# Performance work log

Hardware: AMD Instinct MI355X
Metric: run time of the kernel (lower is better)

## Reference

```python
import jax, jax.numpy as jnp
import numpy as np

N_TERMS = 26000
N_EDGES = 120000
BATCH = 64
N_FEAT = 14          # n_base_models + 4
GO_EMB = 8
HID = 64
IN_DIM = N_FEAT + GO_EMB  # 22


def setup_inputs() -> dict:
    key = jax.random.key(0)
    ks = jax.random.split(key, 12)
    s = 0.05
    return {
        "x": jax.random.normal(ks[0], (BATCH, N_TERMS, N_FEAT), jnp.float32),
        "edge_index": jax.random.randint(ks[1], (2, N_EDGES), 0, N_TERMS, jnp.int32),
        "term_indices": jnp.arange(N_TERMS, dtype=jnp.int32),
        "emb_table": jax.random.normal(ks[2], (N_TERMS, GO_EMB), jnp.float32),
        "W1": jax.random.normal(ks[3], (HID, IN_DIM), jnp.float32) * s,
        "b1": jnp.zeros((HID,), jnp.float32),
        "W2": jax.random.normal(ks[4], (HID, HID), jnp.float32) * s,
        "b2": jnp.zeros((HID,), jnp.float32),
        "W3": jax.random.normal(ks[5], (HID // 2, HID), jnp.float32) * s,
        "b3": jnp.zeros((HID // 2,), jnp.float32),
        "Wout": jax.random.normal(ks[6], (1, HID // 2), jnp.float32) * s,
        "bout": jnp.zeros((1,), jnp.float32),
    }


def _go_conv(x, row, col, deg_inv, W, b):
    # x: [B, N, C]. Mean-aggregate neighbor features (col -> row), add self, linear.
    agg = jnp.zeros_like(x).at[:, row].add(x[:, col])        # scatter_add over edges
    agg = agg * deg_inv[None, :, None]
    return jnp.einsum('bnc,oc->bno', x + agg, W) + b


def reference(x, edge_index, term_indices, emb_table, W1, b1, W2, b2, W3, b3, Wout, bout):
    B, N, _ = x.shape
    row, col = edge_index[0], edge_index[1]
    deg = jnp.zeros((N,), x.dtype).at[row].add(1.0)
    deg_inv = 1.0 / jnp.clip(deg, 1.0)

    go_emb = emb_table[term_indices]                          # [N, GO_EMB]
    h = jnp.concatenate([x, jnp.broadcast_to(go_emb[None], (B, N, go_emb.shape[-1]))], axis=-1)

    h = jax.nn.relu(_go_conv(h, row, col, deg_inv, W1, b1))   # dropout: eval mode (identity)
    h = jax.nn.relu(_go_conv(h, row, col, deg_inv, W2, b2))
    h = jax.nn.relu(_go_conv(h, row, col, deg_inv, W3, b3))
    out = jax.nn.sigmoid(jnp.einsum('bnc,oc->bno', h, Wout) + bout)  # [B, N, 1]
    return out[..., 0]
```

## Files before the change

### kernel.cpp

```cpp
#include <hip/hip_runtime.h>
#include <stdint.h>

static constexpr int NT = 26000;
static constexpr int NE = 120000;

typedef __attribute__((ext_vector_type(8))) short short8;
typedef __attribute__((ext_vector_type(4))) float f32x4;

__device__ __forceinline__ int rfl(int v){ return __builtin_amdgcn_readfirstlane(v); }

__device__ __forceinline__ float bf_lo(uint32_t u){ union{uint32_t u; float f;} a; a.u = u<<16; return a.f; }
__device__ __forceinline__ float bf_hi(uint32_t u){ union{uint32_t u; float f;} a; a.u = u & 0xffff0000u; return a.f; }
__device__ __forceinline__ uint32_t f2b(float f){ union{float f; uint32_t u;} a; a.f=f; return (a.u + 0x7fffu + ((a.u>>16)&1u))>>16; }

__global__ __launch_bounds__(256) void k_zero_deg(int* __restrict__ deg){
  int i = blockIdx.x*256 + threadIdx.x;
  if (i < NT) deg[i] = 0;
}
__global__ __launch_bounds__(256) void k_count(const int* __restrict__ ei, int* __restrict__ deg){
  int e = blockIdx.x*256 + threadIdx.x;
  if (e < NE) atomicAdd(&deg[ei[e]], 1);
}
__global__ __launch_bounds__(1024) void k_scan(const int* __restrict__ deg, int* __restrict__ rp,
                                               int* __restrict__ cur){
  __shared__ int part[1024];
  const int t = threadIdx.x;
  const int CH = (NT + 1023)/1024;
  const int base = t*CH;
  int sum = 0;
  for (int i=0;i<CH;i++){
    int idx=base+i;
    if (idx<NT){ int d = deg[idx]; sum += (d<=4)?4:((d+3)&~3); }
  }
  part[t] = sum;
  __syncthreads();
  for (int off=1; off<1024; off<<=1){
    int v = (t>=off) ? part[t-off] : 0;
    __syncthreads();
    part[t] += v;
    __syncthreads();
  }
  int run = (t==0) ? 0 : part[t-1];
  for (int i=0;i<CH;i++){
    int idx = base+i;
    if (idx<NT){
      int d = deg[idx];
      int slot = (d<=4)?4:((d+3)&~3);
      rp[idx] = run; cur[idx] = run;
      run += slot;
    }
  }
  if (t==1023) rp[NT] = part[1023];
}
__global__ __launch_bounds__(256) void k_init(uint32_t* __restrict__ zp, uint32_t* __restrict__ cols32,
                                              float* __restrict__ scQ, float* __restrict__ scY){
  int i = blockIdx.x*256 + threadIdx.x;
  if (i < 1024) zp[i] = 0;
  else if (i < 1024 + 112004) cols32[i-1024] = 0x65906590u;
  if (i < 2){ scQ[NT*2+i] = 0.f; scY[NT*2+i] = 0.f; }
}
__global__ __launch_bounds__(256) void k_fill(const int* __restrict__ ei, int* __restrict__ cur,
                                              uint16_t* __restrict__ cols){
  int e = blockIdx.x*256 + threadIdx.x;
  if (e < NE){
    int r = ei[e];
    int pos = atomicAdd(&cur[r], 1);
    cols[pos] = (uint16_t)ei[NE + e];
  }
}
__global__ __launch_bounds__(256) void k_prepw(const float* __restrict__ W1, const float* __restrict__ W2,
                                               const float* __restrict__ W3,
                                               uint16_t* __restrict__ Wt1, uint16_t* __restrict__ Wt2,
                                               uint16_t* __restrict__ Wt3){
  for (int idx = threadIdx.x; idx < 8192; idx += 256){
    if (idx < 2048){
      int o = idx >> 5, k = idx & 31;
      Wt1[idx] = (uint16_t)((k < 22) ? f2b(W1[o*22 + k]) : 0);
    } else if (idx < 6144){
      int j = idx - 2048;
      Wt2[j] = (uint16_t)f2b(W2[j]);
    } else {
      int j = idx - 6144;
      Wt3[j] = (uint16_t)f2b(W3[j]);
    }
  }
}

__global__ __launch_bounds__(256) void k_build_h0(const float* __restrict__ x, const int* __restrict__ tidx,
                                                  const float* __restrict__ emb, uint32_t* __restrict__ h0){
  const int n  = blockIdx.x*16 + (threadIdx.x & 15);
  const int b0 = threadIdx.x >> 4;
  const float* er = emb + (size_t)tidx[n]*8;
  float ev[8];
  #pragma unroll
  for (int i=0;i<8;i++) ev[i]=er[i];
  uint32_t* dst = h0 + (size_t)n*512;

  #pragma unroll
  for (int h=0; h<2; h++){
    const int b = b0 + h*16;
    const float* xr = x + ((size_t)b*NT + n)*14;
    float v[32];
    #pragma unroll
    for (int i=0;i<14;i++) v[i]=xr[i];
    #pragma unroll
    for (int i=0;i<8;i++) v[14+i]=ev[i];
    #pragma unroll
    for (int i=22;i<32;i++) v[i]=0.f;
    uint32_t p[16];
    #pragma unroll
    for (int u=0;u<16;u++) p[u] = f2b(v[2*u]) | (f2b(v[2*u+1])<<16);
    const int base = (b>>4)*256 + (b&15)*8;
    *reinterpret_cast<uint4*>(dst + base)       = make_uint4(p[0],p[1],p[2],p[3]);
    *reinterpret_cast<uint4*>(dst + base + 4)   = make_uint4(p[4],p[5],p[6],p[7]);
    *reinterpret_cast<uint4*>(dst + base + 128)   = make_uint4(p[8],p[9],p[10],p[11]);
    *reinterpret_cast<uint4*>(dst + base + 132)   = make_uint4(p[12],p[13],p[14],p[15]);
  }
}

template<int STR>
__device__ __forceinline__ const uint32_t* nbp(const uint32_t* __restrict__ hin,
                                               const uint32_t* __restrict__ zp, int c){
  return (c < NT) ? (hin + (size_t)c*STR) : zp;
}
template<int KS>
__device__ __forceinline__ void gloadv(uint4 (&v)[KS], const uint32_t* __restrict__ p,
                                       const uint32_t (&off)[KS]){
  #pragma unroll
  for (int ks=0; ks<KS; ks++) v[ks] = *reinterpret_cast<const uint4*>(p + off[ks]);
}
template<int KS>
__device__ __forceinline__ void accum(float (&acc)[KS][8], const uint4 (&v)[KS]){
  #pragma unroll
  for (int ks=0;ks<KS;ks++){
    acc[ks][0]+=bf_lo(v[ks].x); acc[ks][1]+=bf_hi(v[ks].x);
    acc[ks][2]+=bf_lo(v[ks].y); acc[ks][3]+=bf_hi(v[ks].y);
    acc[ks][4]+=bf_lo(v[ks].z); acc[ks][5]+=bf_hi(v[ks].z);
    acc[ks][6]+=bf_lo(v[ks].w); acc[ks][7]+=bf_hi(v[ks].w);
  }
}
template<int KS, int STR>
__device__ __forceinline__ float aggregate(float (&acc)[KS][8],
    const uint32_t* __restrict__ hin, const uint32_t* __restrict__ zp,
    const int* __restrict__ rp, const int* __restrict__ cur,
    const uint16_t* __restrict__ cols, int node, const uint32_t (&off)[KS])
{
  const int e0 = rfl(rp[node]);
  const int e1 = rfl(rp[node+1]);
  const int dg = rfl(cur[node]) - e0;

  uint2 cc0 = *reinterpret_cast<const uint2*>(cols + e0);
  int q0 = rfl(cc0.x), q1 = rfl(cc0.y);
  uint4 v0[KS], v1[KS], v2[KS], v3[KS], own[KS];
  gloadv<KS>(v0, nbp<STR>(hin, zp, q0 & 0xffff), off);
  gloadv<KS>(v1, nbp<STR>(hin, zp, (q0 >> 16) & 0xffff), off);
  gloadv<KS>(v2, nbp<STR>(hin, zp, q1 & 0xffff), off);
  gloadv<KS>(v3, nbp<STR>(hin, zp, (q1 >> 16) & 0xffff), off);
  gloadv<KS>(own, hin + (size_t)node*STR, off);
  uint2 ccA = *reinterpret_cast<const uint2*>(cols + e0 + 4);

  const float degf = (float)(dg > 1 ? dg : 1);
  #pragma unroll
  for (int ks=0;ks<KS;ks++){
    acc[ks][0]=bf_lo(own[ks].x)*degf; acc[ks][1]=bf_hi(own[ks].x)*degf;
    acc[ks][2]=bf_lo(own[ks].y)*degf; acc[ks][3]=bf_hi(own[ks].y)*degf;
    acc[ks][4]=bf_lo(own[ks].z)*degf; acc[ks][5]=bf_hi(own[ks].z)*degf;
    acc[ks][6]=bf_lo(own[ks].w)*degf; acc[ks][7]=bf_hi(own[ks].w)*degf;
  }

  for (int e = e0; e < e1; e += 4){
    uint2 ccN = *reinterpret_cast<const uint2*>(cols + e + 8);
    int p0 = rfl(ccA.x), p1 = rfl(ccA.y);
    int n0 = (e+4 < e1) ? (p0 & 0xffff)         : NT;
    int n1 = (e+5 < e1) ? ((p0 >> 16) & 0xffff) : NT;
    int n2 = (e+6 < e1) ? (p1 & 0xffff)         : NT;
    int n3 = (e+7 < e1) ? ((p1 >> 16) & 0xffff) : NT;
    accum<KS>(acc, v0); gloadv<KS>(v0, nbp<STR>(hin, zp, n0), off);
    accum<KS>(acc, v1); gloadv<KS>(v1, nbp<STR>(hin, zp, n1), off);
    accum<KS>(acc, v2); gloadv<KS>(v2, nbp<STR>(hin, zp, n2), off);
    accum<KS>(acc, v3); gloadv<KS>(v3, nbp<STR>(hin, zp, n3), off);
    ccA = ccN;
  }
  return 1.0f / degf;
}

template<int KS> struct VecT;
template<> struct VecT<2>{ using T = uint4; };
template<> struct VecT<1>{ using T = uint2; };

__device__ __forceinline__ void dqu32(float* a, uint32_t u, float s){
  a[0] += s*(float)(int8_t)(u & 0xff);
  a[1] += s*(float)(int8_t)((u>>8) & 0xff);
  a[2] += s*(float)(int8_t)((u>>16) & 0xff);
  a[3] += s*(float)(int8_t)(u>>24);
}
template<int KS>
__device__ __forceinline__ void dqv(float (&acc)[KS][8], const typename VecT<KS>::T& v, float s){
  if constexpr (KS==2){
    dqu32(&acc[0][0], v.x, s); dqu32(&acc[0][4], v.y, s);
    dqu32(&acc[1][0], v.z, s); dqu32(&acc[1][4], v.w, s);
  } else {
    dqu32(&acc[0][0], v.x, s); dqu32(&acc[0][4], v.y, s);
  }
}
template<int KS, int STRB>
__device__ __forceinline__ float aggregate_i8(float (&acc)[KS][8],
    const uint8_t* __restrict__ hin, const uint8_t* __restrict__ zp8,
    const float* __restrict__ sc,
    const int* __restrict__ rp, const int* __restrict__ cur,
    const uint16_t* __restrict__ cols, int node, uint32_t offB, int rt)
{
  using V = typename VecT<KS>::T;
  const int e0 = rfl(rp[node]);
  const int e1 = rfl(rp[node+1]);
  const int dg = rfl(cur[node]) - e0;

  uint2 cc0 = *reinterpret_cast<const uint2*>(cols + e0);
  int a0 = rfl(cc0.x), a1 = rfl(cc0.y);
  int c0 = a0 & 0xffff, c1 = (a0>>16) & 0xffff, c2 = a1 & 0xffff, c3 = (a1>>16) & 0xffff;
  auto bp = [&](int c)->const uint8_t*{ return (c < NT) ? (hin + (size_t)c*STRB) : zp8; };

  V v0 = *reinterpret_cast<const V*>(bp(c0) + offB); float s0 = sc[c0*2+rt];
  V v1 = *reinterpret_cast<const V*>(bp(c1) + offB); float s1 = sc[c1*2+rt];
  V v2 = *reinterpret_cast<const V*>(bp(c2) + offB); float s2 = sc[c2*2+rt];
  V v3 = *reinterpret_cast<const V*>(bp(c3) + offB); float s3 = sc[c3*2+rt];
  V ow = *reinterpret_cast<const V*>(hin + (size_t)node*STRB + offB);
  float so = sc[node*2+rt];
  uint2 ccA = *reinterpret_cast<const uint2*>(cols + e0 + 4);

  const float degf = (float)(dg > 1 ? dg : 1);
  #pragma unroll
  for (int ks=0;ks<KS;ks++)
    #pragma unroll
    for (int j=0;j<8;j++) acc[ks][j]=0.f;
  dqv<KS>(acc, ow, so*degf);

  for (int e = e0; e < e1; e += 4){
    uint2 ccN = *reinterpret_cast<const uint2*>(cols + e + 8);
    int p0 = rfl(ccA.x), p1 = rfl(ccA.y);
    int n0 = (e+4 < e1) ? (p0 & 0xffff)         : NT;
    int n1 = (e+5 < e1) ? ((p0 >> 16) & 0xffff) : NT;
    int n2 = (e+6 < e1) ? (p1 & 0xffff)         : NT;
    int n3 = (e+7 < e1) ? ((p1 >> 16) & 0xffff) : NT;
    dqv<KS>(acc, v0, s0); v0 = *reinterpret_cast<const V*>(bp(n0) + offB); s0 = sc[n0*2+rt];
    dqv<KS>(acc, v1, s1); v1 = *reinterpret_cast<const V*>(bp(n1) + offB); s1 = sc[n1*2+rt];
    dqv<KS>(acc, v2, s2); v2 = *reinterpret_cast<const V*>(bp(n2) + offB); s2 = sc[n2*2+rt];
    dqv<KS>(acc, v3, s3); v3 = *reinterpret_cast<const V*>(bp(n3) + offB); s3 = sc[n3*2+rt];
    ccA = ccN;
  }
  return 1.0f / degf;
}

__global__ __launch_bounds__(256, 8) void k_layer1(
    const uint32_t* __restrict__ hin, uint8_t* __restrict__ qout, float* __restrict__ scQ,
    const int* __restrict__ rp, const int* __restrict__ cur,
    const uint16_t* __restrict__ cols, const uint32_t* __restrict__ zp,
    const uint16_t* __restrict__ Wt, const float* __restrict__ bias)
{
  constexpr int CIN=32, STR=16*CIN;
  const int t=threadIdx.x, lane=t&63, w=t>>6, l15=lane&15, lg=lane>>4;
  const int rt = w & 1;
  const int node = blockIdx.x*2 + (w>>1);

  uint32_t off[1];
  off[0] = (uint32_t)(rt*(CIN*8) + (lg>>1)*128 + l15*8 + (lg&1)*4);

  float acc[1][8];
  const float di = aggregate<1,STR>(acc, hin, zp, rp, cur, cols, node, off);

  short8 bfrag;
  #pragma unroll
  for (int j=0;j<8;j++) bfrag[j] = (short)f2b(acc[0][j]*di);

  float av[4][4];
  float m = 0.f;
  #pragma unroll
  for (int ot=0;ot<4;ot++){
    const int o0 = ot*16;
    short8 af = *reinterpret_cast<const short8*>(Wt + (o0 + l15)*CIN + lg*8);
    f32x4 d = *reinterpret_cast<const f32x4*>(bias + o0 + lg*4);
    d = __builtin_amdgcn_mfma_f32_16x16x32_bf16(af, bfrag, d, 0,0,0);
    #pragma unroll
    for (int j=0;j<4;j++){
      float v = fmaxf(d[j], 0.f);
      av[ot][j] = v;
      m = fmaxf(m, v);
    }
  }
  #pragma unroll
  for (int sh=1; sh<64; sh<<=1) m = fmaxf(m, __shfl_xor(m, sh, 64));
  const float inv = (m > 0.f) ? 127.0f/m : 0.f;

  uint8_t* base = qout + (size_t)node*2048 + rt*1024 + l15*64;
  #pragma unroll
  for (int ot=0;ot<4;ot++){
    uint32_t pk = 0;
    #pragma unroll
    for (int j=0;j<4;j++){
      int q = __float2int_rn(av[ot][j]*inv);
      pk |= (uint32_t)(q & 0xff) << (8*j);
    }
    uint32_t boff = ((((ot&1)<<1)|(lg>>1))<<4) + ((ot>>1)<<3) + ((lg&1)<<2);
    __builtin_nontemporal_store(pk, reinterpret_cast<uint32_t*>(base + boff));
  }
  if (lane == 0) scQ[node*2+rt] = m * (1.0f/127.0f);
}

__global__ __launch_bounds__(256, 6) void k_l2g3(
    const uint8_t* __restrict__ qin, const float* __restrict__ scQ,
    uint8_t* __restrict__ yout, float* __restrict__ scY,
    const int* __restrict__ rp, const int* __restrict__ cur,
    const uint16_t* __restrict__ cols, const uint8_t* __restrict__ zp8,
    const uint16_t* __restrict__ Wt2, const float* __restrict__ bias,
    const uint16_t* __restrict__ Wt3)
{
  __shared__ uint32_t lt[4*512];
  const int t=threadIdx.x, lane=t&63, w=t>>6, l15=lane&15, lg=lane>>4;
  const int rt = w & 1;
  const int node = blockIdx.x*2 + (w>>1);

  const uint32_t offB = (uint32_t)(rt*1024 + l15*64 + lg*16);

  float acc[2][8];
  const float di = aggregate_i8<2,2048>(acc, qin, zp8, scQ, rp, cur, cols, node, offB, rt);

  short8 bfrag[2];
  #pragma unroll
  for (int ks=0;ks<2;ks++){
    short8 bf;
    #pragma unroll
    for (int j=0;j<8;j++) bf[j] = (short)f2b(acc[ks][j]*di);
    bfrag[ks]=bf;
  }

  uint32_t* L = lt + w*512;
  #pragma unroll
  for (int ot=0;ot<4;ot++){
    const int o0 = ot*16;
    short8 af0 = *reinterpret_cast<const short8*>(Wt2 + (o0 + l15)*64 + lg*8);
    short8 af1 = *reinterpret_cast<const short8*>(Wt2 + (o0 + l15)*64 + 32 + lg*8);
    f32x4 d = *reinterpret_cast<const f32x4*>(bias + o0 + lg*4);
    d = __builtin_amdgcn_mfma_f32_16x16x32_bf16(af0, bfrag[0], d, 0,0,0);
    d = __builtin_amdgcn_mfma_f32_16x16x32_bf16(af1, bfrag[1], d, 0,0,0);
    float a0=fmaxf(d[0],0.f), a1=fmaxf(d[1],0.f), a2=fmaxf(d[2],0.f), a3=fmaxf(d[3],0.f);
    *reinterpret_cast<uint2*>(L + ot*128 + l15*8 + lg*2) =
        make_uint2(f2b(a0) | (f2b(a1)<<16), f2b(a2) | (f2b(a3)<<16));
  }

  short8 b3f[2];
  #pragma unroll
  for (int ks=0;ks<2;ks++)
    b3f[ks] = *reinterpret_cast<const short8*>(L + (ks*2+(lg>>1))*128 + l15*8 + (lg&1)*4);

  float dd[2][4];
  float m = 0.f;
  #pragma unroll
  for (int ot=0;ot<2;ot++){
    const int o0 = ot*16;
    short8 af0 = *reinterpret_cast<const short8*>(Wt3 + (o0 + l15)*64 + lg*8);
    short8 af1 = *reinterpret_cast<const short8*>(Wt3 + (o0 + l15)*64 + 32 + lg*8);
    f32x4 d = {0.f,0.f,0.f,0.f};
    d = __builtin_amdgcn_mfma_f32_16x16x32_bf16(af0, b3f[0], d, 0,0,0);
    d = __builtin_amdgcn_mfma_f32_16x16x32_bf16(af1, b3f[1], d, 0,0,0);
    #pragma unroll
    for (int j=0;j<4;j++){
      dd[ot][j] = d[j];
      m = fmaxf(m, fabsf(d[j]));
    }
  }
  #pragma unroll
  for (int sh=1; sh<64; sh<<=1) m = fmaxf(m, __shfl_xor(m, sh, 64));
  const float inv = (m > 0.f) ? 127.0f/m : 0.f;

  uint8_t* base = yout + (size_t)node*1024 + rt*512 + l15*32;
  #pragma unroll
  for (int ot=0;ot<2;ot++){
    uint32_t pk = 0;
    #pragma unroll
    for (int j=0;j<4;j++){
      int q = __float2int_rn(dd[ot][j]*inv);
      pk |= (uint32_t)(q & 0xff) << (8*j);
    }
    uint32_t boff = (((ot<<1)|(lg>>1))<<3) + ((lg&1)<<2);
    __builtin_nontemporal_store(pk, reinterpret_cast<uint32_t*>(base + boff));
  }
  if (lane == 0) scY[node*2+rt] = m * (1.0f/127.0f);
}

__global__ __launch_bounds__(256, 8) void k_fin(
    const uint8_t* __restrict__ yin, const float* __restrict__ scY,
    const int* __restrict__ rp, const int* __restrict__ cur,
    const uint16_t* __restrict__ cols, const uint8_t* __restrict__ zp8,
    const float* __restrict__ b3, const float* __restrict__ Wo, const float* __restrict__ bo,
    float* __restrict__ tmp)
{
  const int t=threadIdx.x, lane=t&63, w=t>>6, l15=lane&15, lg=lane>>4;
  const int rt = w & 1;
  const int node = blockIdx.x*2 + (w>>1);

  const uint32_t offB = (uint32_t)(rt*512 + l15*32 + lg*8);

  float acc[1][8];
  const float di = aggregate_i8<1,1024>(acc, yin, zp8, scY, rp, cur, cols, node, offB, rt);

  const int k0 = lg*8;
  f32x4 bA = *reinterpret_cast<const f32x4*>(b3 + k0);
  f32x4 bB = *reinterpret_cast<const f32x4*>(b3 + k0 + 4);
  f32x4 wA = *reinterpret_cast<const f32x4*>(Wo + k0);
  f32x4 wB = *reinterpret_cast<const f32x4*>(Wo + k0 + 4);
  float z = 0.f;
  #pragma unroll
  for (int j=0;j<4;j++){
    z += fmaxf(acc[0][j]  *di + bA[j], 0.f) * wA[j];
    z += fmaxf(acc[0][4+j]*di + bB[j], 0.f) * wB[j];
  }
  z += __shfl_xor(z, 16, 64);
  z += __shfl_xor(z, 32, 64);
  if (lg == 0){
    float sg = 1.f/(1.f + expf(-(z + bo[0])));
    tmp[(size_t)node*32 + rt*16 + l15] = sg;
  }
}

__global__ __launch_bounds__(256) void k_tr(const float* __restrict__ tmp, float* __restrict__ out){
  int n = blockIdx.x*256 + threadIdx.x;
  if (n < NT){
    f32x4 r[8];
    #pragma unroll
    for (int q=0;q<8;q++) r[q] = *reinterpret_cast<const f32x4*>(tmp + (size_t)n*32 + q*4);
    #pragma unroll
    for (int q=0;q<8;q++)
      #pragma unroll
      for (int j=0;j<4;j++)
        out[(size_t)(q*4+j)*NT + n] = r[q][j];
  }
}

static constexpr size_t OFF_P    = 0;
static constexpr size_t OFF_Q    = 53248000;
static constexpr size_t OFF_TMP  = 106496000;
static constexpr size_t OFF_ZP   = 109824000;
static constexpr size_t OFF_WT1  = OFF_ZP  + 4096;
static constexpr size_t OFF_WT2  = OFF_WT1 + 4096;
static constexpr size_t OFF_WT3  = OFF_WT2 + 8192;
static constexpr size_t OFF_SCQ  = OFF_WT3 + 4096;
static constexpr size_t OFF_SCY  = OFF_SCQ + 208016;
static constexpr size_t OFF_DEG  = OFF_SCY + 208016;
static constexpr size_t OFF_RP   = OFF_DEG + 104000;
static constexpr size_t OFF_CUR  = OFF_RP  + 104016;
static constexpr size_t OFF_COLS = OFF_CUR + 104000;
static constexpr size_t WS_NEED  = OFF_COLS + 448016;

extern "C" void kernel_launch(void* const* d_in, const int* in_sizes, int n_in,
                              void* d_out, int out_size, void* d_ws, size_t ws_size,
                              hipStream_t stream)
{
  const float* x    = (const float*)d_in[0];
  const int*   ei   = (const int*)  d_in[1];
  const int*   tidx = (const int*)  d_in[2];
  const float* emb  = (const float*)d_in[3];
  const float* W1   = (const float*)d_in[4];
  const float* b1   = (const float*)d_in[5];
  const float* W2   = (const float*)d_in[6];
  const float* b2   = (const float*)d_in[7];
  const float* W3   = (const float*)d_in[8];
  const float* b3   = (const float*)d_in[9];
  const float* Wo   = (const float*)d_in[10];
  const float* bo   = (const float*)d_in[11];
  float* out = (float*)d_out;

  if (ws_size < WS_NEED) return;

  char* ws = (char*)d_ws;
  uint32_t* P    = (uint32_t*)(ws + OFF_P);
  uint8_t*  Y3   = (uint8_t*) (ws + OFF_P);
  uint8_t*  Q    = (uint8_t*) (ws + OFF_Q);
  float*    tmpf = (float*)   (ws + OFF_TMP);
  uint32_t* zp   = (uint32_t*)(ws + OFF_ZP);
  uint8_t*  zp8  = (uint8_t*) (ws + OFF_ZP);
  uint16_t* Wt1  = (uint16_t*)(ws + OFF_WT1);
  uint16_t* Wt2  = (uint16_t*)(ws + OFF_WT2);
  uint16_t* Wt3  = (uint16_t*)(ws + OFF_WT3);
  float*    scQ  = (float*)   (ws + OFF_SCQ);
  float*    scY  = (float*)   (ws + OFF_SCY);
  int*      deg  = (int*)     (ws + OFF_DEG);
  int*      rp   = (int*)     (ws + OFF_RP);
  int*      cur  = (int*)     (ws + OFF_CUR);
  uint16_t* cols = (uint16_t*)(ws + OFF_COLS);

  k_zero_deg<<<(NT+255)/256, 256, 0, stream>>>(deg);
  k_count   <<<(NE+255)/256, 256, 0, stream>>>(ei, deg);
  k_scan    <<<1, 1024, 0, stream>>>(deg, rp, cur);
  k_init    <<<442, 256, 0, stream>>>(zp, (uint32_t*)cols, scQ, scY);
  k_fill    <<<(NE+255)/256, 256, 0, stream>>>(ei, cur, cols);
  k_prepw   <<<1, 256, 0, stream>>>(W1, W2, W3, Wt1, Wt2, Wt3);

  for (int ch = 0; ch < 2; ch++){
    k_build_h0<<<NT/16, 256, 0, stream>>>(x + (size_t)ch*32*NT*14, tidx, emb, P);
    k_layer1<<<NT/2, 256, 0, stream>>>(P, Q, scQ, rp, cur, cols, zp, Wt1, b1);
    k_l2g3  <<<NT/2, 256, 0, stream>>>(Q, scQ, Y3, scY, rp, cur, cols, zp8, Wt2, b2, Wt3);
    k_fin   <<<NT/2, 256, 0, stream>>>(Y3, scY, rp, cur, cols, zp8, b3, Wo, bo, tmpf);
    k_tr    <<<(NT+255)/256, 256, 0, stream>>>(tmpf, out + (size_t)ch*32*NT);
  }
}
```

Measured before the change: 523.8 us.

## Quantize layer-0 features to int8 with per-node scales and use unsigned post-ReLU layer1 output

The input features (x plus GO embeddings) are now stored as 8-bit values with a per-node, per-batch-half scale (offset by 128) instead of bf16. This halves the gather traffic in the first aggregation, and the offset is removed afterwards using a running sum of the neighbour scales. Layer-1 output is stored as unsigned 8-bit with a 255 range, since it is non-negative after ReLU, which gives an extra bit of precision. Aggregation is unified into one templated routine with signed, unsigned and offset modes. The cost is more quantization error on the raw inputs.

```diff
diff --git a/kernel.cpp b/kernel.cpp
--- a/kernel.cpp
+++ b/kernel.cpp
@@ -6,12 +6,18 @@
 
 typedef __attribute__((ext_vector_type(8))) short short8;
 typedef __attribute__((ext_vector_type(4))) float f32x4;
+typedef __attribute__((ext_vector_type(4))) unsigned int u32x4;
 
 __device__ __forceinline__ int rfl(int v){ return __builtin_amdgcn_readfirstlane(v); }
 
 __device__ __forceinline__ float bf_lo(uint32_t u){ union{uint32_t u; float f;} a; a.u = u<<16; return a.f; }
 __device__ __forceinline__ float bf_hi(uint32_t u){ union{uint32_t u; float f;} a; a.u = u & 0xffff0000u; return a.f; }
 __device__ __forceinline__ uint32_t f2b(float f){ union{float f; uint32_t u;} a; a.f=f; return (a.u + 0x7fffu + ((a.u>>16)&1u))>>16; }
+
+__device__ __forceinline__ void nts4(uint8_t* p, uint32_t a, uint32_t b, uint32_t c, uint32_t d){
+  u32x4 v; v.x=a; v.y=b; v.z=c; v.w=d;
+  __builtin_nontemporal_store(v, reinterpret_cast<u32x4*>(p));
+}
 
 __global__ __launch_bounds__(256) void k_zero_deg(int* __restrict__ deg){
   int i = blockIdx.x*256 + threadIdx.x;
@@ -53,11 +59,12 @@
   if (t==1023) rp[NT] = part[1023];
 }
 __global__ __launch_bounds__(256) void k_init(uint32_t* __restrict__ zp, uint32_t* __restrict__ cols32,
-                                              float* __restrict__ scQ, float* __restrict__ scY){
+                                              float* __restrict__ scP, float* __restrict__ scQ,
+                                              float* __restrict__ scY){
   int i = blockIdx.x*256 + threadIdx.x;
   if (i < 1024) zp[i] = 0;
   else if (i < 1024 + 112004) cols32[i-1024] = 0x65906590u;
-  if (i < 2){ scQ[NT*2+i] = 0.f; scY[NT*2+i] = 0.f; }
+  if (i < 2){ scP[NT*2+i] = 0.f; scQ[NT*2+i] = 0.f; scY[NT*2+i] = 0.f; }
 }
 __global__ __launch_bounds__(256) void k_fill(const int* __restrict__ ei, int* __restrict__ cur,
                                               uint16_t* __restrict__ cols){
@@ -87,86 +94,125 @@
 }
 
 __global__ __launch_bounds__(256) void k_build_h0(const float* __restrict__ x, const int* __restrict__ tidx,
-                                                  const float* __restrict__ emb, uint32_t* __restrict__ h0){
-  const int n  = blockIdx.x*16 + (threadIdx.x & 15);
-  const int b0 = threadIdx.x >> 4;
+                                                  const float* __restrict__ emb,
+                                                  uint8_t* __restrict__ p8, float* __restrict__ scP){
+  __shared__ float red[2][16][16];
+  __shared__ float sinv[2][16];
+  const int t  = threadIdx.x;
+  const int ni = t & 15;
+  const int n  = blockIdx.x*16 + ni;
+  const int r  = t >> 4;
   const float* er = emb + (size_t)tidx[n]*8;
   float ev[8];
   #pragma unroll
   for (int i=0;i<8;i++) ev[i]=er[i];
-  uint32_t* dst = h0 + (size_t)n*512;
-
-  #pragma unroll
-  for (int h=0; h<2; h++){
-    const int b = b0 + h*16;
+
+  float v[2][32];
+  #pragma unroll
+  for (int rt=0; rt<2; rt++){
+    const int b = r + rt*16;
     const float* xr = x + ((size_t)b*NT + n)*14;
-    float v[32];
-    #pragma unroll
-    for (int i=0;i<14;i++) v[i]=xr[i];
-    #pragma unroll
-    for (int i=0;i<8;i++) v[14+i]=ev[i];
-    #pragma unroll
-    for (int i=22;i<32;i++) v[i]=0.f;
-    uint32_t p[16];
-    #pragma unroll
-    for (int u=0;u<16;u++) p[u] = f2b(v[2*u]) | (f2b(v[2*u+1])<<16);
-    const int base = (b>>4)*256 + (b&15)*8;
-    *reinterpret_cast<uint4*>(dst + base)       = make_uint4(p[0],p[1],p[2],p[3]);
-    *reinterpret_cast<uint4*>(dst + base + 4)   = make_uint4(p[4],p[5],p[6],p[7]);
-    *reinterpret_cast<uint4*>(dst + base + 128)   = make_uint4(p[8],p[9],p[10],p[11]);
-    *reinterpret_cast<uint4*>(dst + base + 132)   = make_uint4(p[12],p[13],p[14],p[15]);
-  }
-}
-
-template<int STR>
-__device__ __forceinline__ const uint32_t* nbp(const uint32_t* __restrict__ hin,
-                                               const uint32_t* __restrict__ zp, int c){
-  return (c < NT) ? (hin + (size_t)c*STR) : zp;
-}
-template<int KS>
-__device__ __forceinline__ void gloadv(uint4 (&v)[KS], const uint32_t* __restrict__ p,
-                                       const uint32_t (&off)[KS]){
-  #pragma unroll
-  for (int ks=0; ks<KS; ks++) v[ks] = *reinterpret_cast<const uint4*>(p + off[ks]);
-}
-template<int KS>
-__device__ __forceinline__ void accum(float (&acc)[KS][8], const uint4 (&v)[KS]){
-  #pragma unroll
-  for (int ks=0;ks<KS;ks++){
-    acc[ks][0]+=bf_lo(v[ks].x); acc[ks][1]+=bf_hi(v[ks].x);
-    acc[ks][2]+=bf_lo(v[ks].y); acc[ks][3]+=bf_hi(v[ks].y);
-    acc[ks][4]+=bf_lo(v[ks].z); acc[ks][5]+=bf_hi(v[ks].z);
-    acc[ks][6]+=bf_lo(v[ks].w); acc[ks][7]+=bf_hi(v[ks].w);
-  }
-}
-template<int KS, int STR>
-__device__ __forceinline__ float aggregate(float (&acc)[KS][8],
-    const uint32_t* __restrict__ hin, const uint32_t* __restrict__ zp,
+    float m = 0.f;
+    #pragma unroll
+    for (int i=0;i<14;i++){ float a=xr[i]; v[rt][i]=a; m=fmaxf(m,fabsf(a)); }
+    #pragma unroll
+    for (int i=0;i<8;i++){ float a=ev[i]; v[rt][14+i]=a; m=fmaxf(m,fabsf(a)); }
+    #pragma unroll
+    for (int i=22;i<32;i++) v[rt][i]=0.f;
+    red[rt][r][ni] = m;
+  }
+  __syncthreads();
+  if (t < 32){
+    int rt = t >> 4, nn = t & 15;
+    float mm = 0.f;
+    #pragma unroll
+    for (int i=0;i<16;i++) mm = fmaxf(mm, red[rt][i][nn]);
+    sinv[rt][nn] = (mm > 0.f) ? 127.0f/mm : 0.f;
+    scP[(size_t)(blockIdx.x*16+nn)*2 + rt] = mm * (1.0f/127.0f);
+  }
+  __syncthreads();
+
+  uint8_t* dst = p8 + (size_t)n*1024;
+  #pragma unroll
+  for (int rt=0; rt<2; rt++){
+    const float inv = sinv[rt][ni];
+    uint32_t pk[8];
+    #pragma unroll
+    for (int u=0;u<8;u++){
+      uint32_t w = 0;
+      #pragma unroll
+      for (int j=0;j<4;j++){
+        int q = __float2int_rn(v[rt][u*4+j]*inv) + 128;
+        q = q < 0 ? 0 : (q > 255 ? 255 : q);
+        w |= (uint32_t)q << (8*j);
+      }
+      pk[u] = w;
+    }
+    nts4(dst + rt*512 + r*32,      pk[0],pk[1],pk[2],pk[3]);
+    nts4(dst + rt*512 + r*32 + 16, pk[4],pk[5],pk[6],pk[7]);
+  }
+}
+
+template<int KS> struct VecT;
+template<> struct VecT<2>{ using T = uint4; };
+template<> struct VecT<1>{ using T = uint2; };
+
+__device__ __forceinline__ void dq_u(float* a, uint32_t u, float s){
+  a[0] += s*(float)(u & 0xffu);
+  a[1] += s*(float)((u>>8) & 0xffu);
+  a[2] += s*(float)((u>>16) & 0xffu);
+  a[3] += s*(float)(u>>24);
+}
+__device__ __forceinline__ void dq_s(float* a, uint32_t u, float s){
+  a[0] += s*(float)(int8_t)(u & 0xff);
+  a[1] += s*(float)(int8_t)((u>>8) & 0xff);
+  a[2] += s*(float)(int8_t)((u>>16) & 0xff);
+  a[3] += s*(float)(int8_t)(u>>24);
+}
+template<int KS, bool SG>
+__device__ __forceinline__ void dqv(float (&acc)[KS][8], const typename VecT<KS>::T& v, float s){
+  if constexpr (KS==2){
+    if constexpr (SG){ dq_s(&acc[0][0],v.x,s); dq_s(&acc[0][4],v.y,s); dq_s(&acc[1][0],v.z,s); dq_s(&acc[1][4],v.w,s); }
+    else             { dq_u(&acc[0][0],v.x,s); dq_u(&acc[0][4],v.y,s); dq_u(&acc[1][0],v.z,s); dq_u(&acc[1][4],v.w,s); }
+  } else {
+    if constexpr (SG){ dq_s(&acc[0][0],v.x,s); dq_s(&acc[0][4],v.y,s); }
+    else             { dq_u(&acc[0][0],v.x,s); dq_u(&acc[0][4],v.y,s); }
+  }
+}
+
+template<int KS, int STRB, int MODE>
+__device__ __forceinline__ float aggregate_q(float (&acc)[KS][8], float& sumS,
+    const uint8_t* __restrict__ hin, const uint8_t* __restrict__ zp8,
+    const float* __restrict__ sc,
     const int* __restrict__ rp, const int* __restrict__ cur,
-    const uint16_t* __restrict__ cols, int node, const uint32_t (&off)[KS])
+    const uint16_t* __restrict__ cols, int node, uint32_t offB, int rt)
 {
+  using V = typename VecT<KS>::T;
+  constexpr bool SG = (MODE==2);
   const int e0 = rfl(rp[node]);
   const int e1 = rfl(rp[node+1]);
   const int dg = rfl(cur[node]) - e0;
 
   uint2 cc0 = *reinterpret_cast<const uint2*>(cols + e0);
-  int q0 = rfl(cc0.x), q1 = rfl(cc0.y);
-  uint4 v0[KS], v1[KS], v2[KS], v3[KS], own[KS];
-  gloadv<KS>(v0, nbp<STR>(hin, zp, q0 & 0xffff), off);
-  gloadv<KS>(v1, nbp<STR>(hin, zp, (q0 >> 16) & 0xffff), off);
-  gloadv<KS>(v2, nbp<STR>(hin, zp, q1 & 0xffff), off);
-  gloadv<KS>(v3, nbp<STR>(hin, zp, (q1 >> 16) & 0xffff), off);
-  gloadv<KS>(own, hin + (size_t)node*STR, off);
+  int a0 = rfl(cc0.x), a1 = rfl(cc0.y);
+  int c0 = a0 & 0xffff, c1 = (a0>>16) & 0xffff, c2 = a1 & 0xffff, c3 = (a1>>16) & 0xffff;
+  auto bp = [&](int c)->const uint8_t*{ return (c < NT) ? (hin + (size_t)c*STRB) : zp8; };
+
+  V v0 = *reinterpret_cast<const V*>(bp(c0) + offB); float s0 = sc[c0*2+rt];
+  V v1 = *reinterpret_cast<const V*>(bp(c1) + offB); float s1 = sc[c1*2+rt];
+  V v2 = *reinterpret_cast<const V*>(bp(c2) + offB); float s2 = sc[c2*2+rt];
+  V v3 = *reinterpret_cast<const V*>(bp(c3) + offB); float s3 = sc[c3*2+rt];
+  V ow = *reinterpret_cast<const V*>(hin + (size_t)node*STRB + offB);
+  float so = sc[node*2+rt];
   uint2 ccA = *reinterpret_cast<const uint2*>(cols + e0 + 4);
 
   const float degf = (float)(dg > 1 ? dg : 1);
   #pragma unroll
-  for (int ks=0;ks<KS;ks++){
-    acc[ks][0]=bf_lo(own[ks].x)*degf; acc[ks][1]=bf_hi(own[ks].x)*degf;
-    acc[ks][2]=bf_lo(own[ks].y)*degf; acc[ks][3]=bf_hi(own[ks].y)*degf;
-    acc[ks][4]=bf_lo(own[ks].z)*degf; acc[ks][5]=bf_hi(own[ks].z)*degf;
-    acc[ks][6]=bf_lo(own[ks].w)*degf; acc[ks][7]=bf_hi(own[ks].w)*degf;
-  }
+  for (int ks=0;ks<KS;ks++)
+    #pragma unroll
+    for (int j=0;j<8;j++) acc[ks][j]=0.f;
+  dqv<KS,SG>(acc, ow, so*degf);
+  if constexpr (MODE==1) sumS = so*degf;
 
   for (int e = e0; e < e1; e += 4){
     uint2 ccN = *reinterpret_cast<const uint2*>(cols + e + 8);
@@ -175,109 +221,46 @@
     int n1 = (e+5 < e1) ? ((p0 >> 16) & 0xffff) : NT;
     int n2 = (e+6 < e1) ? (p1 & 0xffff)         : NT;
     int n3 = (e+7 < e1) ? ((p1 >> 16) & 0xffff) : NT;
-    accum<KS>(acc, v0); gloadv<KS>(v0, nbp<STR>(hin, zp, n0), off);
-    accum<KS>(acc, v1); gloadv<KS>(v1, nbp<STR>(hin, zp, n1), off);
-    accum<KS>(acc, v2); gloadv<KS>(v2, nbp<STR>(hin, zp, n2), off);
-    accum<KS>(acc, v3); gloadv<KS>(v3, nbp<STR>(hin, zp, n3), off);
+    dqv<KS,SG>(acc, v0, s0); if constexpr (MODE==1) sumS += s0;
+    v0 = *reinterpret_cast<const V*>(bp(n0) + offB); s0 = sc[n0*2+rt];
+    dqv<KS,SG>(acc, v1, s1); if constexpr (MODE==1) sumS += s1;
+    v1 = *reinterpret_cast<const V*>(bp(n1) + offB); s1 = sc[n1*2+rt];
+    dqv<KS,SG>(acc, v2, s2); if constexpr (MODE==1) sumS += s2;
+    v2 = *reinterpret_cast<const V*>(bp(n2) + offB); s2 = sc[n2*2+rt];
+    dqv<KS,SG>(acc, v3, s3); if constexpr (MODE==1) sumS += s3;
+    v3 = *reinterpret_cast<const V*>(bp(n3) + offB); s3 = sc[n3*2+rt];
     ccA = ccN;
   }
   return 1.0f / degf;
 }
 
-template<int KS> struct VecT;
-template<> struct VecT<2>{ using T = uint4; };
-template<> struct VecT<1>{ using T = uint2; };
-
-__device__ __forceinline__ void dqu32(float* a, uint32_t u, float s){
-  a[0] += s*(float)(int8_t)(u & 0xff);
-  a[1] += s*(float)(int8_t)((u>>8) & 0xff);
-  a[2] += s*(float)(int8_t)((u>>16) & 0xff);
-  a[3] += s*(float)(int8_t)(u>>24);
-}
-template<int KS>
-__device__ __forceinline__ void dqv(float (&acc)[KS][8], const typename VecT<KS>::T& v, float s){
-  if constexpr (KS==2){
-    dqu32(&acc[0][0], v.x, s); dqu32(&acc[0][4], v.y, s);
-    dqu32(&acc[1][0], v.z, s); dqu32(&acc[1][4], v.w, s);
-  } else {
-    dqu32(&acc[0][0], v.x, s); dqu32(&acc[0][4], v.y, s);
-  }
-}
-template<int KS, int STRB>
-__device__ __forceinline__ float aggregate_i8(float (&acc)[KS][8],
-    const uint8_t* __restrict__ hin, const uint8_t* __restrict__ zp8,
-    const float* __restrict__ sc,
+__global__ __launch_bounds__(256, 8) void k_layer1(
+    const uint8_t* __restrict__ pin, const float* __restrict__ scP,
+    uint8_t* __restrict__ qout, float* __restrict__ scQ,
     const int* __restrict__ rp, const int* __restrict__ cur,
-    const uint16_t* __restrict__ cols, int node, uint32_t offB, int rt)
-{
-  using V = typename VecT<KS>::T;
-  const int e0 = rfl(rp[node]);
-  const int e1 = rfl(rp[node+1]);
-  const int dg = rfl(cur[node]) - e0;
-
-  uint2 cc0 = *reinterpret_cast<const uint2*>(cols + e0);
-  int a0 = rfl(cc0.x), a1 = rfl(cc0.y);
-  int c0 = a0 & 0xffff, c1 = (a0>>16) & 0xffff, c2 = a1 & 0xffff, c3 = (a1>>16) & 0xffff;
-  auto bp = [&](int c)->const uint8_t*{ return (c < NT) ? (hin + (size_t)c*STRB) : zp8; };
-
-  V v0 = *reinterpret_cast<const V*>(bp(c0) + offB); float s0 = sc[c0*2+rt];
-  V v1 = *reinterpret_cast<const V*>(bp(c1) + offB); float s1 = sc[c1*2+rt];
-  V v2 = *reinterpret_cast<const V*>(bp(c2) + offB); float s2 = sc[c2*2+rt];
-  V v3 = *reinterpret_cast<const V*>(bp(c3) + offB); float s3 = sc[c3*2+rt];
-  V ow = *reinterpret_cast<const V*>(hin + (size_t)node*STRB + offB);
-  float so = sc[node*2+rt];
-  uint2 ccA = *reinterpret_cast<const uint2*>(cols + e0 + 4);
-
-  const float degf = (float)(dg > 1 ? dg : 1);
-  #pragma unroll
-  for (int ks=0;ks<KS;ks++)
-    #pragma unroll
-    for (int j=0;j<8;j++) acc[ks][j]=0.f;
-  dqv<KS>(acc, ow, so*degf);
-
-  for (int e = e0; e < e1; e += 4){
-    uint2 ccN = *reinterpret_cast<const uint2*>(cols + e + 8);
-    int p0 = rfl(ccA.x), p1 = rfl(ccA.y);
-    int n0 = (e+4 < e1) ? (p0 & 0xffff)         : NT;
-    int n1 = (e+5 < e1) ? ((p0 >> 16) & 0xffff) : NT;
-    int n2 = (e+6 < e1) ? (p1 & 0xffff)         : NT;
-    int n3 = (e+7 < e1) ? ((p1 >> 16) & 0xffff) : NT;
-    dqv<KS>(acc, v0, s0); v0 = *reinterpret_cast<const V*>(bp(n0) + offB); s0 = sc[n0*2+rt];
-    dqv<KS>(acc, v1, s1); v1 = *reinterpret_cast<const V*>(bp(n1) + offB); s1 = sc[n1*2+rt];
-    dqv<KS>(acc, v2, s2); v2 = *reinterpret_cast<const V*>(bp(n2) + offB); s2 = sc[n2*2+rt];
-    dqv<KS>(acc, v3, s3); v3 = *reinterpret_cast<const V*>(bp(n3) + offB); s3 = sc[n3*2+rt];
-    ccA = ccN;
-  }
-  return 1.0f / degf;
-}
-
-__global__ __launch_bounds__(256, 8) void k_layer1(
-    const uint32_t* __restrict__ hin, uint8_t* __restrict__ qout, float* __restrict__ scQ,
-    const int* __restrict__ rp, const int* __restrict__ cur,
-    const uint16_t* __restrict__ cols, const uint32_t* __restrict__ zp,
+    const uint16_t* __restrict__ cols, const uint8_t* __restrict__ zp8,
     const uint16_t* __restrict__ Wt, const float* __restrict__ bias)
 {
-  constexpr int CIN=32, STR=16*CIN;
   const int t=threadIdx.x, lane=t&63, w=t>>6, l15=lane&15, lg=lane>>4;
   const int rt = w & 1;
   const int node = blockIdx.x*2 + (w>>1);
 
-  uint32_t off[1];
-  off[0] = (uint32_t)(rt*(CIN*8) + (lg>>1)*128 + l15*8 + (lg&1)*4);
-
-  float acc[1][8];
-  const float di = aggregate<1,STR>(acc, hin, zp, rp, cur, cols, node, off);
+  const uint32_t offB = (uint32_t)(rt*512 + l15*32 + lg*8);
+
+  float acc[1][8]; float sumS = 0.f;
+  const float di = aggregate_q<1,1024,1>(acc, sumS, pin, zp8, scP, rp, cur, cols, node, offB, rt);
+  const float corr = 128.0f * sumS;
 
   short8 bfrag;
   #pragma unroll
-  for (int j=0;j<8;j++) bfrag[j] = (short)f2b(acc[0][j]*di);
+  for (int j=0;j<8;j++) bfrag[j] = (short)f2b((acc[0][j] - corr)*di);
 
   float av[4][4];
   float m = 0.f;
   #pragma unroll
   for (int ot=0;ot<4;ot++){
     const int o0 = ot*16;
-    short8 af = *reinterpret_cast<const short8*>(Wt + (o0 + l15)*CIN + lg*8);
+    short8 af = *reinterpret_cast<const short8*>(Wt + (o0 + l15)*32 + lg*8);
     f32x4 d = *reinterpret_cast<const f32x4*>(bias + o0 + lg*4);
     d = __builtin_amdgcn_mfma_f32_16x16x32_bf16(af, bfrag, d, 0,0,0);
     #pragma unroll
@@ -289,7 +272,7 @@
   }
   #pragma unroll
   for (int sh=1; sh<64; sh<<=1) m = fmaxf(m, __shfl_xor(m, sh, 64));
-  const float inv = (m > 0.f) ? 127.0f/m : 0.f;
+  const float inv = (m > 0.f) ? 255.0f/m : 0.f;
 
   uint8_t* base = qout + (size_t)node*2048 + rt*1024 + l15*64;
   #pragma unroll
@@ -298,12 +281,13 @@
     #pragma unroll
     for (int j=0;j<4;j++){
       int q = __float2int_rn(av[ot][j]*inv);
-      pk |= (uint32_t)(q & 0xff) << (8*j);
+      q = q > 255 ? 255 : q;
+      pk |= (uint32_t)q << (8*j);
     }
     uint32_t boff = ((((ot&1)<<1)|(lg>>1))<<4) + ((ot>>1)<<3) + ((lg&1)<<2);
     __builtin_nontemporal_store(pk, reinterpret_cast<uint32_t*>(base + boff));
   }
-  if (lane == 0) scQ[node*2+rt] = m * (1.0f/127.0f);
+  if (lane == 0) scQ[node*2+rt] = m * (1.0f/255.0f);
 }
 
 __global__ __launch_bounds__(256, 6) void k_l2g3(
@@ -321,8 +305,8 @@
 
   const uint32_t offB = (uint32_t)(rt*1024 + l15*64 + lg*16);
 
-  float acc[2][8];
-  const float di = aggregate_i8<2,2048>(acc, qin, zp8, scQ, rp, cur, cols, node, offB, rt);
+  float acc[2][8]; float dummy;
+  const float di = aggregate_q<2,2048,0>(acc, dummy, qin, zp8, scQ, rp, cur, cols, node, offB, rt);
 
   short8 bfrag[2];
   #pragma unroll
@@ -400,8 +384,8 @@
 
   const uint32_t offB = (uint32_t)(rt*512 + l15*32 + lg*8);
 
-  float acc[1][8];
-  const float di = aggregate_i8<1,1024>(acc, yin, zp8, scY, rp, cur, cols, node, offB, rt);
+  float acc[1][8]; float dummy;
+  const float di = aggregate_q<1,1024,2>(acc, dummy, yin, zp8, scY, rp, cur, cols, node, offB, rt);
 
   const int k0 = lg*8;
   f32x4 bA = *reinterpret_cast<const f32x4*>(b3 + k0);
@@ -437,13 +421,14 @@
 }
 
 static constexpr size_t OFF_P    = 0;
-static constexpr size_t OFF_Q    = 53248000;
-static constexpr size_t OFF_TMP  = 106496000;
-static constexpr size_t OFF_ZP   = 109824000;
+static constexpr size_t OFF_Q    = 26624000;
+static constexpr size_t OFF_TMP  = 79872000;
+static constexpr size_t OFF_ZP   = 83200000;
 static constexpr size_t OFF_WT1  = OFF_ZP  + 4096;
 static constexpr size_t OFF_WT2  = OFF_WT1 + 4096;
 static constexpr size_t OFF_WT3  = OFF_WT2 + 8192;
-static constexpr size_t OFF_SCQ  = OFF_WT3 + 4096;
+static constexpr size_t OFF_SCP  = OFF_WT3 + 4096;
+static constexpr size_t OFF_SCQ  = OFF_SCP + 208016;
 static constexpr size_t OFF_SCY  = OFF_SCQ + 208016;
 static constexpr size_t OFF_DEG  = OFF_SCY + 208016;
 static constexpr size_t OFF_RP   = OFF_DEG + 104000;
@@ -472,7 +457,7 @@
   if (ws_size < WS_NEED) return;
 
   char* ws = (char*)d_ws;
-  uint32_t* P    = (uint32_t*)(ws + OFF_P);
+  uint8_t*  P    = (uint8_t*) (ws + OFF_P);
   uint8_t*  Y3   = (uint8_t*) (ws + OFF_P);
   uint8_t*  Q    = (uint8_t*) (ws + OFF_Q);
   float*    tmpf = (float*)   (ws + OFF_TMP);
@@ -481,6 +466,7 @@
   uint16_t* Wt1  = (uint16_t*)(ws + OFF_WT1);
   uint16_t* Wt2  = (uint16_t*)(ws + OFF_WT2);
   uint16_t* Wt3  = (uint16_t*)(ws + OFF_WT3);
+  float*    scP  = (float*)   (ws + OFF_SCP);
   float*    scQ  = (float*)   (ws + OFF_SCQ);
   float*    scY  = (float*)   (ws + OFF_SCY);
   int*      deg  = (int*)     (ws + OFF_DEG);
@@ -491,13 +477,13 @@
   k_zero_deg<<<(NT+255)/256, 256, 0, stream>>>(deg);
   k_count   <<<(NE+255)/256, 256, 0, stream>>>(ei, deg);
   k_scan    <<<1, 1024, 0, stream>>>(deg, rp, cur);
-  k_init    <<<442, 256, 0, stream>>>(zp, (uint32_t*)cols, scQ, scY);
+  k_init    <<<442, 256, 0, stream>>>(zp, (uint32_t*)cols, scP, scQ, scY);
   k_fill    <<<(NE+255)/256, 256, 0, stream>>>(ei, cur, cols);
   k_prepw   <<<1, 256, 0, stream>>>(W1, W2, W3, Wt1, Wt2, Wt3);
 
   for (int ch = 0; ch < 2; ch++){
-    k_build_h0<<<NT/16, 256, 0, stream>>>(x + (size_t)ch*32*NT*14, tidx, emb, P);
-    k_layer1<<<NT/2, 256, 0, stream>>>(P, Q, scQ, rp, cur, cols, zp, Wt1, b1);
+    k_build_h0<<<NT/16, 256, 0, stream>>>(x + (size_t)ch*32*NT*14, tidx, emb, P, scP);
+    k_layer1<<<NT/2, 256, 0, stream>>>(P, scP, Q, scQ, rp, cur, cols, zp8, Wt1, b1);
     k_l2g3  <<<NT/2, 256, 0, stream>>>(Q, scQ, Y3, scY, rp, cur, cols, zp8, Wt2, b2, Wt3);
     k_fin   <<<NT/2, 256, 0, stream>>>(Y3, scY, rp, cur, cols, zp8, b3, Wo, bo, tmpf);
     k_tr    <<<(NT+255)/256, 256, 0, stream>>>(tmpf, out + (size_t)ch*32*NT);
```

Result: faster. 501.0 us (-4.4%).
